# Kernel tuning notes

Measured on AMD Instinct MI355X. Metric: run time of the kernel, lower is better.

Reference implementation:

```python
import jax, jax.numpy as jnp
import numpy as np

VOCAB, DIM, LAYERS = 32000, 1024, 4
B, L = 8, 512


def setup_inputs() -> dict:
    key = jax.random.key(0)
    ks = jax.random.split(key, 8)
    s = 0.02
    return {
        "input_ids": jax.random.randint(ks[0], (B, L), 0, VOCAB),
        "embed_W": jax.random.normal(ks[1], (VOCAB, DIM), jnp.float32) * s,
        "h_starter": jax.random.normal(ks[2], (LAYERS, DIM), jnp.float32) * s,
        "gate_W": jax.random.normal(ks[3], (LAYERS, 2 * DIM, 2 * DIM), jnp.float32) * s,
        "gate_b": jnp.zeros((LAYERS, 2 * DIM), jnp.float32),
        "cand_W": jax.random.normal(ks[4], (LAYERS, DIM, 2 * DIM), jnp.float32) * s,
        "cand_b": jnp.zeros((LAYERS, DIM), jnp.float32),
        "out_W": jax.random.normal(ks[5], (VOCAB, DIM), jnp.float32) * s,
    }


def _gru_forward(input_ids, embed_W, h_starter, gate_W, gate_b, cand_W, cand_b, out_W):
    Bsz = input_ids.shape[0]
    x = embed_W[input_ids]                      # [B, L, D]
    h0 = jnp.broadcast_to(h_starter[:, None, :], (LAYERS, Bsz, DIM))  # [Ly, B, D]

    def step(h, x_t):
        # h: [Ly, B, D], x_t: [B, D]
        new_h = []
        xin = x_t
        for i in range(LAYERS):
            hi = h[i]
            xh = jnp.concatenate([xin, hi], axis=-1)           # [B, 2D]
            g = xh @ gate_W[i].T + gate_b[i]                   # [B, 2D]
            z, r = jnp.split(g, 2, axis=-1)
            z = jax.nn.sigmoid(z)
            r = jax.nn.sigmoid(r)
            cin = jnp.concatenate([xin, r * hi], axis=-1)      # [B, 2D]
            cand = jnp.tanh(cin @ cand_W[i].T + cand_b[i])     # [B, D]
            hn = z * hi + (1.0 - z) * cand
            new_h.append(hn)
            xin = hn
        return jnp.stack(new_h), xin

    _, ys = jax.lax.scan(step, h0, jnp.swapaxes(x, 0, 1))      # ys: [L, B, D]
    ys = jnp.swapaxes(ys, 0, 1)                                # [B, L, D]
    logits = jnp.einsum('bld,vd->blv', ys, out_W)              # [B, L, V]
    return logits


def reference(input_ids, embed_W, h_starter, gate_W, gate_b, cand_W, cand_b, out_W):
    return _gru_forward(input_ids, embed_W, h_starter, gate_W, gate_b, cand_W, cand_b, out_W)
```

## Files before the change

kernel.cpp:

```cpp
#include <hip/hip_runtime.h>
#include <hip/hip_bf16.h>

#define VOCAB  32000
#define DIM    1024
#define NLAYER 4
#define NB     8
#define SEQ    512

#define NGROUP       4
#define GBLKS        64
#define SCAN_BLOCKS  (NGROUP * GBLKS)
#define SCAN_THREADS 512
#define ROWH         2056

typedef __attribute__((ext_vector_type(8))) short          bf16x8;
typedef __attribute__((ext_vector_type(4))) float          f32x4;
typedef __attribute__((ext_vector_type(2))) float          f32x2;
typedef __attribute__((ext_vector_type(8))) unsigned short u16x8;
typedef __attribute__((ext_vector_type(4))) unsigned short u16x4;
typedef __attribute__((ext_vector_type(8))) _Float16       h8f;
typedef __attribute__((ext_vector_type(4))) _Float16       h4f;

__device__ __forceinline__ u16x8 cvt8_bf16(const float* p) {
    float4 f0 = *(const float4*)p;
    float4 f1 = *(const float4*)(p + 4);
    union { __hip_bfloat16 h[8]; u16x8 v; } u;
    u.h[0] = __float2bfloat16(f0.x); u.h[1] = __float2bfloat16(f0.y);
    u.h[2] = __float2bfloat16(f0.z); u.h[3] = __float2bfloat16(f0.w);
    u.h[4] = __float2bfloat16(f1.x); u.h[5] = __float2bfloat16(f1.y);
    u.h[6] = __float2bfloat16(f1.z); u.h[7] = __float2bfloat16(f1.w);
    return u.v;
}

__device__ __forceinline__ h8f pack8(f32x4 a, f32x4 b) {
    h8f o;
    o[0] = (_Float16)a[0]; o[1] = (_Float16)a[1];
    o[2] = (_Float16)a[2]; o[3] = (_Float16)a[3];
    o[4] = (_Float16)b[0]; o[5] = (_Float16)b[1];
    o[6] = (_Float16)b[2]; o[7] = (_Float16)b[3];
    return o;
}

__device__ __forceinline__ void ld4v(f32x4& d, const float* p) {
    asm volatile("global_load_dwordx4 %0, %1, off sc0 sc1"
                 : "=&v"(d) : "v"(p));
}
__device__ __forceinline__ void st8v(void* p, f32x2 v) {
    asm volatile("global_store_dwordx2 %0, %1, off sc0 sc1"
                 :: "v"(p), "v"(v) : "memory");
}
__device__ __forceinline__ void st2v(void* p, unsigned v) {
    asm volatile("global_store_short %0, %1, off sc0 sc1"
                 :: "v"(p), "v"(v) : "memory");
}
__device__ __forceinline__ void vmwait0() {
    asm volatile("s_waitcnt vmcnt(0)" ::: "memory");
}

__global__ void bar_init_kernel(unsigned* __restrict__ bar) {
    bar[threadIdx.x]        = 0u;
    bar[threadIdx.x + 1024] = 0u;
    bar[threadIdx.x + 2048] = 0u;
    bar[threadIdx.x + 3072] = 0u;
}

__device__ __forceinline__ void slot_bar(unsigned* __restrict__ slots, int bkg,
                                         unsigned seq, bool& dead) {
    __syncthreads();
    const int tid = threadIdx.x;
    if (tid == 0)
        __hip_atomic_store(&slots[bkg * 8], seq, __ATOMIC_RELAXED,
                           __HIP_MEMORY_SCOPE_AGENT);
    if (tid < 64 && !dead) {
        unsigned guard = 0;
        for (;;) {
            unsigned v = __hip_atomic_load(&slots[tid * 8], __ATOMIC_RELAXED,
                                           __HIP_MEMORY_SCOPE_AGENT);
            if (__all((int)(v >= seq))) break;
            __builtin_amdgcn_s_sleep(1);
            if (++guard > (1u << 16)) { dead = true; break; }
        }
    }
    __syncthreads();
}

__global__ void __launch_bounds__(SCAN_THREADS)
__attribute__((amdgpu_waves_per_eu(2, 2)))
gru_scan(
    const int*   __restrict__ ids,
    const float* __restrict__ embW,
    const float* __restrict__ hstart,
    const float* __restrict__ gW,
    const float* __restrict__ gB,
    const float* __restrict__ cW,
    const float* __restrict__ cB,
    _Float16* __restrict__ hbuf16,
    _Float16* __restrict__ rbuf16,
    __hip_bfloat16* __restrict__ ysfb,
    unsigned* __restrict__ bar)
{
    __shared__ _Float16 act[NB][ROWH];
    __shared__ float pz[4][4][64];
    __shared__ float pr[4][4][64];
    __shared__ float pc[2][4][64];
    __shared__ float pcb[2][4][64];
    __shared__ float hb[4][64];

    const int tid   = threadIdx.x;
    const int lane  = tid & 63;
    const int wv    = tid >> 6;
    const int l15   = lane & 15;
    const int lgq   = lane >> 4;
    const int bcol  = l15 & 7;
    const int g     = blockIdx.x >> 6;
    const int bkg   = blockIdx.x & (GBLKS-1);
    const int jbase = bkg * 16;
    const int jrow  = jbase + l15;

    h8f Wa[16], Wb[16];
    if (wv < 6) {
        const float* wzp = gW + ((size_t)g * 2048 + jrow) * 2048;
        const float* wrp = gW + ((size_t)g * 2048 + 1024 + jrow) * 2048;
        const float* wcp = cW + ((size_t)g * 1024 + jrow) * 2048;
        const float* baseA; const float* baseB; int koA, koB;
        switch (wv) {
          case 0:  baseA = wzp; koA = 0;    baseB = wrp; koB = 0;    break;
          case 1:  baseA = wzp; koA = 512;  baseB = wrp; koB = 512;  break;
          case 2:  baseA = wzp; koA = 1024; baseB = wrp; koB = 1024; break;
          case 3:  baseA = wzp; koA = 1536; baseB = wrp; koB = 1536; break;
          case 4:  baseA = wcp; koA = 0;    baseB = wcp; koB = 1024; break;
          default: baseA = wcp; koA = 512;  baseB = wcp; koB = 1536; break;
        }
        #pragma unroll
        for (int kc = 0; kc < 16; ++kc) {
            const int ka = koA + kc * 32 + lgq * 8;
            const int kb = koB + kc * 32 + lgq * 8;
            Wa[kc] = pack8(*(const f32x4*)(baseA + ka), *(const f32x4*)(baseA + ka + 4));
            Wb[kc] = pack8(*(const f32x4*)(baseB + kb), *(const f32x4*)(baseB + kb + 4));
        }
        #pragma unroll
        for (int kc = 0; kc < 16; ++kc) {
            asm volatile("" : "+v"(Wa[kc]));
            asm volatile("" : "+v"(Wb[kc]));
        }
    }

    float bz4[4], br4[4], cb4[4], hold[4], zreg[4];
    if (wv == 6) {
        #pragma unroll
        for (int r = 0; r < 4; ++r) {
            const int j = jbase + lgq * 4 + r;
            bz4[r]  = gB[g * 2048 + j];
            cb4[r]  = cB[g * 1024 + j];
            hold[r] = hstart[g * 1024 + j];
            hb[r][lane] = hold[r];
        }
    }
    if (wv == 7) {
        #pragma unroll
        for (int r = 0; r < 4; ++r)
            br4[r] = gB[g * 2048 + 1024 + jbase + lgq * 4 + r];
    }

    bool dead = false;
    unsigned* slots1g = bar + g * 512;
    unsigned* slots2g = bar + 2048 + g * 512;
    unsigned* s2prev  = (g > 0)          ? bar + 2048 + (g - 1) * 512 : nullptr;
    unsigned* s1next  = (g < NGROUP - 1) ? bar + (g + 1) * 512        : nullptr;
    _Float16* rbufg16 = rbuf16 + (size_t)g * NB * DIM;

    if (tid < 128) {
        int e = bkg * 128 + tid;
        union { _Float16 h; unsigned short u; } cv;
        cv.h = (_Float16)hstart[g * DIM + (e & (DIM - 1))];
        st2v(&hbuf16[((size_t)3 * NLAYER + g) * NB * DIM + e], (unsigned)cv.u);
    }
    slot_bar(slots2g, bkg, 1u, dead);

    for (int t = 0; t < SEQ; ++t) {
        const int so = (t + 3) & 3;
        const int sw = t & 3;
        const _Float16* hsrc16  = hbuf16 + ((size_t)so * NLAYER + g) * NB * DIM;
        _Float16*       hdst16  = hbuf16 + ((size_t)sw * NLAYER + g) * NB * DIM;
        const _Float16* xprev16 = hbuf16 + ((size_t)sw * NLAYER + (g > 0 ? g - 1 : 0)) * NB * DIM;

        {
            const unsigned need_a = (g > 0) ? (unsigned)(t + 2) : 0u;
            const unsigned need_b = (g < NGROUP - 1 && t >= 4) ? (unsigned)(t - 3) : 0u;
            if (tid < 64 && !dead && (need_a | need_b)) {
                unsigned guard = 0;
                for (;;) {
                    bool ok = true;
                    if (need_a)
                        ok &= (__hip_atomic_load(&s2prev[tid * 8], __ATOMIC_RELAXED,
                                                 __HIP_MEMORY_SCOPE_AGENT) >= need_a);
                    if (need_b)
                        ok &= (__hip_atomic_load(&s1next[tid * 8], __ATOMIC_RELAXED,
                                                 __HIP_MEMORY_SCOPE_AGENT) >= need_b);
                    if (__all((int)ok)) break;
                    __builtin_amdgcn_s_sleep(1);
                    if (++guard > (1u << 16)) { dead = true; break; }
                }
            }
            __syncthreads();
        }

        if (g == 0) {
            #pragma unroll
            for (int q = 0; q < 2; ++q) {
                const int u = q * SCAN_THREADS + tid;
                const int b = u >> 7, d8 = (u & 127) * 8;
                const float* p = embW + (size_t)ids[b * SEQ + t] * DIM + d8;
                *(h8f*)&act[b][d8] = pack8(*(const f32x4*)p, *(const f32x4*)(p + 4));
            }
            f32x4 hv[2];
            #pragma unroll
            for (int q = 0; q < 2; ++q) {
                const int u = q * SCAN_THREADS + tid;
                ld4v(hv[q], (const float*)(hsrc16 + (size_t)(u >> 7) * DIM + (u & 127) * 8));
            }
            vmwait0();
            asm volatile("" : "+v"(hv[0]), "+v"(hv[1]));
            #pragma unroll
            for (int q = 0; q < 2; ++q) {
                const int u = q * SCAN_THREADS + tid;
                *(h8f*)&act[u >> 7][1024 + (u & 127) * 8] = __builtin_bit_cast(h8f, hv[q]);
            }
        } else {
            f32x4 xv[2], hv[2];
            #pragma unroll
            for (int q = 0; q < 2; ++q) {
                const int u = q * SCAN_THREADS + tid;
                ld4v(xv[q], (const float*)(xprev16 + (size_t)(u >> 7) * DIM + (u & 127) * 8));
                ld4v(hv[q], (const float*)(hsrc16 + (size_t)(u >> 7) * DIM + (u & 127) * 8));
            }
            vmwait0();
            asm volatile("" : "+v"(xv[0]), "+v"(xv[1]), "+v"(hv[0]), "+v"(hv[1]));
            #pragma unroll
            for (int q = 0; q < 2; ++q) {
                const int u = q * SCAN_THREADS + tid;
                const int b = u >> 7, d8 = (u & 127) * 8;
                *(h8f*)&act[b][d8]        = __builtin_bit_cast(h8f, xv[q]);
                *(h8f*)&act[b][1024 + d8] = __builtin_bit_cast(h8f, hv[q]);
            }
        }
        __syncthreads();

        if (wv < 6) {
            const int kb2 = (wv < 4) ? wv * 512 : (wv - 4) * 512;
            f32x4 accA = {0.f, 0.f, 0.f, 0.f};
            f32x4 accB = {0.f, 0.f, 0.f, 0.f};
            #pragma unroll
            for (int kc = 0; kc < 16; ++kc) {
                const h8f bf = *(const h8f*)&act[bcol][kb2 + kc * 32 + lgq * 8];
                accA = __builtin_amdgcn_mfma_f32_16x16x32_f16(Wa[kc], bf, accA, 0, 0, 0);
                if (wv < 4)
                    accB = __builtin_amdgcn_mfma_f32_16x16x32_f16(Wb[kc], bf, accB, 0, 0, 0);
            }
            if (wv < 4) {
                #pragma unroll
                for (int r = 0; r < 4; ++r) {
                    pz[wv][r][lane] = accA[r];
                    pr[wv][r][lane] = accB[r];
                }
            } else {
                #pragma unroll
                for (int r = 0; r < 4; ++r) pc[wv - 4][r][lane] = accA[r];
            }
        }
        __syncthreads();

        if (wv == 6) {
            #pragma unroll
            for (int r = 0; r < 4; ++r) {
                const float s = pz[0][r][lane] + pz[1][r][lane]
                              + pz[2][r][lane] + pz[3][r][lane] + bz4[r];
                zreg[r] = 1.f / (1.f + expf(-s));
            }
        }
        if (wv == 7) {
            h4f rh4;
            #pragma unroll
            for (int r = 0; r < 4; ++r) {
                const float s = pr[0][r][lane] + pr[1][r][lane]
                              + pr[2][r][lane] + pr[3][r][lane] + br4[r];
                const float rg = 1.f / (1.f + expf(-s));
                rh4[r] = (_Float16)(rg * hb[r][lane]);
            }
            if (l15 < 8)
                st8v(rbufg16 + (size_t)bcol * DIM + jbase + lgq * 4,
                     __builtin_bit_cast(f32x2, rh4));
        }
        slot_bar(slots1g, bkg, (unsigned)(t + 1), dead);

        {
            f32x4 rv[2];
            #pragma unroll
            for (int q = 0; q < 2; ++q) {
                const int u = q * SCAN_THREADS + tid;
                ld4v(rv[q], (const float*)(rbufg16 + (size_t)(u >> 7) * DIM + (u & 127) * 8));
            }
            vmwait0();
            asm volatile("" : "+v"(rv[0]), "+v"(rv[1]));
            #pragma unroll
            for (int q = 0; q < 2; ++q) {
                const int u = q * SCAN_THREADS + tid;
                *(h8f*)&act[u >> 7][(u & 127) * 8] = __builtin_bit_cast(h8f, rv[q]);
            }
        }
        __syncthreads();

        if (wv == 4 || wv == 5) {
            const int kb2 = (wv - 4) * 512;
            f32x4 acc = {0.f, 0.f, 0.f, 0.f};
            #pragma unroll
            for (int kc = 0; kc < 16; ++kc) {
                const h8f bf = *(const h8f*)&act[bcol][kb2 + kc * 32 + lgq * 8];
                acc = __builtin_amdgcn_mfma_f32_16x16x32_f16(Wb[kc], bf, acc, 0, 0, 0);
            }
            #pragma unroll
            for (int r = 0; r < 4; ++r) pcb[wv - 4][r][lane] = acc[r];
        }
        __syncthreads();

        if (wv == 6) {
            h4f hp; u16x4 yp;
            #pragma unroll
            for (int r = 0; r < 4; ++r) {
                const float cand = tanhf(pc[0][r][lane] + pc[1][r][lane]
                                         + pcb[0][r][lane] + pcb[1][r][lane] + cb4[r]);
                const float hn = zreg[r] * hold[r] + (1.f - zreg[r]) * cand;
                hold[r] = hn;
                hb[r][lane] = hn;
                hp[r] = (_Float16)hn;
                union { __hip_bfloat16 b; unsigned short u; } cv;
                cv.b = __float2bfloat16(hn);
                yp[r] = cv.u;
            }
            if (l15 < 8) {
                st8v(hdst16 + (size_t)bcol * DIM + jbase + lgq * 4,
                     __builtin_bit_cast(f32x2, hp));
                if (g == NGROUP - 1)
                    *(f32x2*)(ysfb + ((size_t)bcol * SEQ + t) * DIM + jbase + lgq * 4) =
                        __builtin_bit_cast(f32x2, yp);
            }
        }
        slot_bar(slots2g, bkg, (unsigned)(t + 2), dead);
    }

    if (dead && tid == 0) {
        union { __hip_bfloat16 b; unsigned short u; } cv;
        cv.b = __float2bfloat16(1.0e8f);
        ((unsigned short*)ysfb)[blockIdx.x] = cv.u;
    }
}

#define BM 128
#define BN 128
#define BK 64

__global__ void __launch_bounds__(256) out_gemm(
    const __hip_bfloat16* __restrict__ A,
    const float* __restrict__ B,
    float* __restrict__ C)
{
    __shared__ __hip_bfloat16 At[BM][BK + 8];
    __shared__ __hip_bfloat16 Bt[BN][BK + 8];

    const int tid  = threadIdx.x;
    const int lane = tid & 63;
    const int wv   = tid >> 6;
    const int wm   = wv >> 1, wn = wv & 1;
    const int m0   = blockIdx.y * BM;
    const int n0   = blockIdx.x * BN;

    f32x4 acc[4][4];
    #pragma unroll
    for (int i = 0; i < 4; ++i)
        #pragma unroll
        for (int jj = 0; jj < 4; ++jj)
            acc[i][jj] = (f32x4){0.f, 0.f, 0.f, 0.f};

    const int srow = tid >> 3;
    const int scol = (tid & 7) * 8;
    const int l15  = lane & 15;
    const int l4   = lane >> 4;

    for (int kt = 0; kt < DIM / BK; ++kt) {
        const int k0 = kt * BK;
        #pragma unroll
        for (int rnd = 0; rnd < 4; ++rnd) {
            const int row = rnd * 32 + srow;
            *(u16x8*)&At[row][scol] =
                *(const u16x8*)&A[(size_t)(m0 + row) * DIM + k0 + scol];
            *(u16x8*)&Bt[row][scol] =
                cvt8_bf16(&B[(size_t)(n0 + row) * DIM + k0 + scol]);
        }
        __syncthreads();
        #pragma unroll
        for (int ks = 0; ks < 2; ++ks) {
            bf16x8 av[4], bv[4];
            #pragma unroll
            for (int i = 0; i < 4; ++i) {
                av[i] = *(const bf16x8*)&At[wm * 64 + i * 16 + l15][ks * 32 + l4 * 8];
                bv[i] = *(const bf16x8*)&Bt[wn * 64 + i * 16 + l15][ks * 32 + l4 * 8];
            }
            #pragma unroll
            for (int i = 0; i < 4; ++i)
                #pragma unroll
                for (int jj = 0; jj < 4; ++jj)
                    acc[i][jj] = __builtin_amdgcn_mfma_f32_16x16x32_bf16(
                        av[i], bv[jj], acc[i][jj], 0, 0, 0);
        }
        __syncthreads();
    }

    const int rq = l4 * 4;
    #pragma unroll
    for (int i = 0; i < 4; ++i) {
        const int rbase = m0 + wm * 64 + i * 16 + rq;
        #pragma unroll
        for (int jj = 0; jj < 4; ++jj) {
            const int col = n0 + wn * 64 + jj * 16 + l15;
            #pragma unroll
            for (int r2 = 0; r2 < 4; ++r2)
                C[(size_t)(rbase + r2) * VOCAB + col] = acc[i][jj][r2];
        }
    }
}

extern "C" void kernel_launch(void* const* d_in, const int* in_sizes, int n_in,
                              void* d_out, int out_size, void* d_ws, size_t ws_size,
                              hipStream_t stream)
{
    (void)in_sizes; (void)n_in; (void)out_size; (void)ws_size;
    const int*   ids  = (const int*)  d_in[0];
    const float* embW = (const float*)d_in[1];
    const float* hst  = (const float*)d_in[2];
    const float* gW   = (const float*)d_in[3];
    const float* gB   = (const float*)d_in[4];
    const float* cW   = (const float*)d_in[5];
    const float* cB   = (const float*)d_in[6];
    const float* outW = (const float*)d_in[7];
    float* logits = (float*)d_out;

    char* ws = (char*)d_ws;
    unsigned*       bar    = (unsigned*)ws;
    _Float16*       rbuf16 = (_Float16*)(ws + 16384);
    _Float16*       hbuf16 = (_Float16*)(ws + 16384 + 65536);
    __hip_bfloat16* ysfb   = (__hip_bfloat16*)(ws + 16384 + 65536 + 262144);

    bar_init_kernel<<<dim3(1), dim3(1024), 0, stream>>>(bar);

    gru_scan<<<dim3(SCAN_BLOCKS), dim3(SCAN_THREADS), 0, stream>>>(
        ids, embW, hst, gW, gB, cW, cB, hbuf16, rbuf16, ysfb, bar);

    out_gemm<<<dim3(VOCAB / BN, (NB * SEQ) / BM), dim3(256), 0, stream>>>(ysfb, outW, logits);
}
```

Measured before the change: 3.694 ms.

## Convert out_W to bf16 inside idle scan blocks, use bf16-bf16 output GEMM

Blocks of the GRU scan that belong to groups beyond the first now convert the fp32 output projection weights to bf16 in workspace before starting their pipelined layer work. This overlaps the conversion with the scan's startup latency. The output GEMM then reads bf16 B directly, which halves its weight traffic and removes per-tile conversion. The conversion delays the start of later-layer groups in the scan pipeline, and the new path only runs when the workspace is large enough.

```diff
diff --git a/kernel.cpp b/kernel.cpp
--- a/kernel.cpp
+++ b/kernel.cpp
@@ -97,7 +97,10 @@
     _Float16* __restrict__ hbuf16,
     _Float16* __restrict__ rbuf16,
     __hip_bfloat16* __restrict__ ysfb,
-    unsigned* __restrict__ bar)
+    unsigned* __restrict__ bar,
+    const float* __restrict__ outW,
+    __hip_bfloat16* __restrict__ outWb,
+    int doConv)
 {
     __shared__ _Float16 act[NB][ROWH];
     __shared__ float pz[4][4][64];
@@ -116,6 +119,12 @@
     const int bkg   = blockIdx.x & (GBLKS-1);
     const int jbase = bkg * 16;
     const int jrow  = jbase + l15;
+
+    if (doConv && g > 0) {
+        const int cidx = (blockIdx.x - GBLKS) * SCAN_THREADS + tid;
+        for (int u = cidx; u < VOCAB * DIM / 8; u += (SCAN_BLOCKS - GBLKS) * SCAN_THREADS)
+            ((u16x8*)outWb)[u] = cvt8_bf16(outW + (size_t)u * 8);
+    }
 
     h8f Wa[16], Wb[16];
     if (wv < 6) {
@@ -359,7 +368,77 @@
 #define BN 128
 #define BK 64
 
-__global__ void __launch_bounds__(256) out_gemm(
+__global__ void __launch_bounds__(256) out_gemm_bb(
+    const __hip_bfloat16* __restrict__ A,
+    const __hip_bfloat16* __restrict__ B,
+    float* __restrict__ C)
+{
+    __shared__ __hip_bfloat16 At[BM][BK + 8];
+    __shared__ __hip_bfloat16 Bt[BN][BK + 8];
+
+    const int tid  = threadIdx.x;
+    const int lane = tid & 63;
+    const int wv   = tid >> 6;
+    const int wm   = wv >> 1, wn = wv & 1;
+    const int m0   = blockIdx.y * BM;
+    const int n0   = blockIdx.x * BN;
+
+    f32x4 acc[4][4];
+    #pragma unroll
+    for (int i = 0; i < 4; ++i)
+        #pragma unroll
+        for (int jj = 0; jj < 4; ++jj)
+            acc[i][jj] = (f32x4){0.f, 0.f, 0.f, 0.f};
+
+    const int srow = tid >> 3;
+    const int scol = (tid & 7) * 8;
+    const int l15  = lane & 15;
+    const int l4   = lane >> 4;
+
+    for (int kt = 0; kt < DIM / BK; ++kt) {
+        const int k0 = kt * BK;
+        #pragma unroll
+        for (int rnd = 0; rnd < 4; ++rnd) {
+            const int row = rnd * 32 + srow;
+            *(u16x8*)&At[row][scol] =
+                *(const u16x8*)&A[(size_t)(m0 + row) * DIM + k0 + scol];
+            *(u16x8*)&Bt[row][scol] =
+                *(const u16x8*)&B[(size_t)(n0 + row) * DIM + k0 + scol];
+        }
+        __syncthreads();
+        #pragma unroll
+        for (int ks = 0; ks < 2; ++ks) {
+            bf16x8 av[4], bv[4];
+            #pragma unroll
+            for (int i = 0; i < 4; ++i) {
+                av[i] = *(const bf16x8*)&At[wm * 64 + i * 16 + l15][ks * 32 + l4 * 8];
+                bv[i] = *(const bf16x8*)&Bt[wn * 64 + i * 16 + l15][ks * 32 + l4 * 8];
+            }
+            #pragma unroll
+            for (int i = 0; i < 4; ++i)
+                #pragma unroll
+                for (int jj = 0; jj < 4; ++jj)
+                    acc[i][jj] = __builtin_amdgcn_mfma_f32_16x16x32_bf16(
+                        av[i], bv[jj], acc[i][jj], 0, 0, 0);
+        }
+        __syncthreads();
+    }
+
+    const int rq = l4 * 4;
+    #pragma unroll
+    for (int i = 0; i < 4; ++i) {
+        const int rbase = m0 + wm * 64 + i * 16 + rq;
+        #pragma unroll
+        for (int jj = 0; jj < 4; ++jj) {
+            const int col = n0 + wn * 64 + jj * 16 + l15;
+            #pragma unroll
+            for (int r2 = 0; r2 < 4; ++r2)
+                C[(size_t)(rbase + r2) * VOCAB + col] = acc[i][jj][r2];
+        }
+    }
+}
+
+__global__ void __launch_bounds__(256) out_gemm_bf(
     const __hip_bfloat16* __restrict__ A,
     const float* __restrict__ B,
     float* __restrict__ C)
@@ -433,7 +512,7 @@
                               void* d_out, int out_size, void* d_ws, size_t ws_size,
                               hipStream_t stream)
 {
-    (void)in_sizes; (void)n_in; (void)out_size; (void)ws_size;
+    (void)in_sizes; (void)n_in; (void)out_size;
     const int*   ids  = (const int*)  d_in[0];
     const float* embW = (const float*)d_in[1];
     const float* hst  = (const float*)d_in[2];
@@ -449,11 +528,21 @@
     _Float16*       rbuf16 = (_Float16*)(ws + 16384);
     _Float16*       hbuf16 = (_Float16*)(ws + 16384 + 65536);
     __hip_bfloat16* ysfb   = (__hip_bfloat16*)(ws + 16384 + 65536 + 262144);
+    const size_t outWb_off = 16384 + 65536 + 262144 + (size_t)NB * SEQ * DIM * 2;
+    const size_t need      = outWb_off + (size_t)VOCAB * DIM * 2;
+    const int doConv = (ws_size >= need) ? 1 : 0;
+    __hip_bfloat16* outWb = doConv ? (__hip_bfloat16*)(ws + outWb_off) : nullptr;
 
     bar_init_kernel<<<dim3(1), dim3(1024), 0, stream>>>(bar);
 
     gru_scan<<<dim3(SCAN_BLOCKS), dim3(SCAN_THREADS), 0, stream>>>(
-        ids, embW, hst, gW, gB, cW, cB, hbuf16, rbuf16, ysfb, bar);
-
-    out_gemm<<<dim3(VOCAB / BN, (NB * SEQ) / BM), dim3(256), 0, stream>>>(ysfb, outW, logits);
-}
+        ids, embW, hst, gW, gB, cW, cB, hbuf16, rbuf16, ysfb, bar,
+        outW, outWb, doConv);
+
+    if (doConv)
+        out_gemm_bb<<<dim3(VOCAB / BN, (NB * SEQ) / BM), dim3(256), 0, stream>>>(
+            ysfb, outWb, logits);
+    else
+        out_gemm_bf<<<dim3(VOCAB / BN, (NB * SEQ) / BM), dim3(256), 0, stream>>>(
+            ysfb, outW, logits);
+}
```

Result: faster. 3.504 ms (-5.2%).
